# Performance work log

Measured on AMD Instinct MI355X. Metric: run time of the kernel, lower is better.

The kernel has to match this reference:

```python
import jax, jax.numpy as jnp
import numpy as np

N_HEAD = 8
D_MODEL = 512
D_K = 64
D_V = 64
LN_EPS = 1e-6


def setup_inputs() -> dict:
    key = jax.random.key(0)
    ks = jax.random.split(key, 8)
    B, L = 4, 1024
    inp = {
        "q": jax.random.normal(ks[0], (B, L, D_MODEL), dtype=jnp.float32),
        "k": jax.random.normal(ks[1], (B, L, D_MODEL), dtype=jnp.float32),
        "v": jax.random.normal(ks[2], (B, L, D_MODEL), dtype=jnp.float32),
        "w_qs": jax.random.normal(ks[3], (D_MODEL, N_HEAD * D_K), dtype=jnp.float32) * 0.02,
        "w_ks": jax.random.normal(ks[4], (D_MODEL, N_HEAD * D_K), dtype=jnp.float32) * 0.02,
        "w_vs": jax.random.normal(ks[5], (D_MODEL, N_HEAD * D_V), dtype=jnp.float32) * 0.02,
        "w_sk": jax.random.normal(ks[6], (D_V, N_HEAD * D_V), dtype=jnp.float32) * 0.02,
        "w_fc": jax.random.normal(ks[7], (D_V, D_MODEL), dtype=jnp.float32) * 0.02,
        "ln_gamma": jnp.ones((D_MODEL,), dtype=jnp.float32),
        "ln_beta": jnp.zeros((D_MODEL,), dtype=jnp.float32),
    }
    return inp


def reference(q, k, v, w_qs, w_ks, w_vs, w_sk, w_fc, ln_gamma, ln_beta):
    B, Lq, _ = q.shape
    Lk = k.shape[1]
    temp = jnp.asarray(D_K ** 0.5, q.dtype)
    residual = q

    # QKV projections (bias=False), split heads: [B, H, L, d]
    qh = (q @ w_qs).reshape(B, Lq, N_HEAD, D_K).transpose(0, 2, 1, 3)
    kh = (k @ w_ks).reshape(B, Lk, N_HEAD, D_K).transpose(0, 2, 1, 3)
    vh = (v @ w_vs).reshape(B, Lk, N_HEAD, D_V).transpose(0, 2, 1, 3)

    # scaled dot-product attention (dropout in eval mode = identity)
    attn = jax.nn.softmax(jnp.einsum('bhqd,bhkd->bhqk', qh / temp, kh), axis=-1)
    o = jnp.einsum('bhqk,bhkd->bhqd', attn, vh)  # [B, H, Lq, D_V]

    # SPA: selective parallel attention head gating
    u = o.sum(axis=1)                       # [B, Lq, D_V]
    s = u.mean(axis=1)                      # adaptive avg pool over Lq -> [B, D_V]
    g = jax.nn.softmax((s @ w_sk).reshape(B, N_HEAD, D_V), axis=1)  # softmax over heads
    f = o * g[:, :, None, :]                # gate each head, broadcast over Lq
    qo = f.sum(axis=1)                      # sum heads -> [B, Lq, D_V]

    # fc + residual + LayerNorm (dropout eval = identity)
    out = qo @ w_fc + residual              # [B, Lq, D_MODEL]
    mu = out.mean(axis=-1, keepdims=True)
    var = out.var(axis=-1, keepdims=True)
    out = (out - mu) * jax.lax.rsqrt(var + LN_EPS) * ln_gamma + ln_beta
    return out, attn
```

## Files before the change

kernel.cpp:

```cpp
#include <hip/hip_runtime.h>
#include <hip/hip_bf16.h>
#include <cstdint>

#define NH 8
#define DM 512
#define DH 64
#define NB 4
#define SL 1024

typedef __attribute__((ext_vector_type(8))) short bf16x8;
typedef __attribute__((ext_vector_type(4))) float f32x4;
typedef __attribute__((ext_vector_type(4))) unsigned int u32x4;

static __device__ __forceinline__ float bf2f(short s) {
  union { unsigned int u; float f; } c;
  c.u = ((unsigned int)(unsigned short)s) << 16;
  return c.f;
}
static __device__ __forceinline__ unsigned short f2bfbits(float f) {
  union { float f; unsigned int u; } c; c.f = f;
  unsigned int lsb = (c.u >> 16) & 1u;
  unsigned int r = c.u + 0x7fffu + lsb;
  return (unsigned short)(r >> 16);
}

__global__ __launch_bounds__(256) void k_cvt_act(
    const float* __restrict__ q, const float* __restrict__ k, const float* __restrict__ v,
    ushort* __restrict__ qb, ushort* __restrict__ kb, ushort* __restrict__ vb) {
  int i = blockIdx.x * 256 + threadIdx.x;
  {
    float4 f = ((const float4*)q)[i];
    ushort4 r = { f2bfbits(f.x), f2bfbits(f.y), f2bfbits(f.z), f2bfbits(f.w) };
    *(ushort4*)(qb + 4 * i) = r;
  }
  {
    float4 f = ((const float4*)k)[i];
    ushort4 r = { f2bfbits(f.x), f2bfbits(f.y), f2bfbits(f.z), f2bfbits(f.w) };
    *(ushort4*)(kb + 4 * i) = r;
  }
  {
    float4 f = ((const float4*)v)[i];
    ushort4 r = { f2bfbits(f.x), f2bfbits(f.y), f2bfbits(f.z), f2bfbits(f.w) };
    *(ushort4*)(vb + 4 * i) = r;
  }
}

__global__ __launch_bounds__(256) void k_cvt_wT(
    const float* __restrict__ w0, const float* __restrict__ w1, const float* __restrict__ w2,
    ushort* __restrict__ o0, ushort* __restrict__ o1, ushort* __restrict__ o2) {
  __shared__ ushort tile[64][65];
  const float* src = blockIdx.z == 0 ? w0 : (blockIdx.z == 1 ? w1 : w2);
  ushort* dst = blockIdx.z == 0 ? o0 : (blockIdx.z == 1 ? o1 : o2);
  int k0 = blockIdx.x * 64, n0 = blockIdx.y * 64;
  int t = threadIdx.x;
  #pragma unroll
  for (int i = 0; i < 16; ++i) {
    int lin = t + i * 256, r = lin >> 6, c = lin & 63;
    tile[r][c] = f2bfbits(src[(size_t)(k0 + r) * DM + n0 + c]);
  }
  __syncthreads();
  #pragma unroll
  for (int i = 0; i < 16; ++i) {
    int lin = t + i * 256, r = lin >> 6, c = lin & 63;
    dst[(size_t)(n0 + r) * DM + k0 + c] = tile[c][r];
  }
}

__global__ __launch_bounds__(256) void k_cvt_wfc(const float* __restrict__ w, ushort* __restrict__ o) {
  int i = blockIdx.x * 256 + threadIdx.x;
  float4 f = ((const float4*)w)[i];
  ushort4 r = { f2bfbits(f.x), f2bfbits(f.y), f2bfbits(f.z), f2bfbits(f.w) };
  *(ushort4*)(o + 4 * i) = r;
}

__global__ __launch_bounds__(256) void k_proj(
    const ushort* __restrict__ qb, const ushort* __restrict__ kb, const ushort* __restrict__ vb,
    const ushort* __restrict__ wqT, const ushort* __restrict__ wkT, const ushort* __restrict__ wvT,
    ushort* __restrict__ Qh, ushort* __restrict__ Kh, ushort* __restrict__ VhT) {
  int z = blockIdx.z;
  const ushort* A = z == 0 ? qb : (z == 1 ? kb : vb);
  const ushort* W = z == 0 ? wqT : (z == 1 ? wkT : wvT);
  ushort* Out = z == 0 ? Qh : (z == 1 ? Kh : VhT);
  float scale = z == 0 ? 0.125f * 1.44269504088896f : 1.0f;

  int wid = threadIdx.x >> 6, l = threadIdx.x & 63;
  int lr = l & 15, lg = l >> 4;
  int row0 = blockIdx.x * 64 + wid * 16;
  int col0 = blockIdx.y * 64;
  const ushort* Arow = A + (size_t)(row0 + lr) * DM + lg * 8;

  f32x4 acc0 = {0.f, 0.f, 0.f, 0.f}, acc1 = acc0, acc2 = acc0, acc3 = acc0;
  #pragma unroll 4
  for (int kt = 0; kt < 16; ++kt) {
    bf16x8 a = *(const bf16x8*)(Arow + kt * 32);
    bf16x8 b0 = *(const bf16x8*)(W + (size_t)(col0 + 0 * 16 + lr) * DM + kt * 32 + lg * 8);
    bf16x8 b1 = *(const bf16x8*)(W + (size_t)(col0 + 1 * 16 + lr) * DM + kt * 32 + lg * 8);
    bf16x8 b2 = *(const bf16x8*)(W + (size_t)(col0 + 2 * 16 + lr) * DM + kt * 32 + lg * 8);
    bf16x8 b3 = *(const bf16x8*)(W + (size_t)(col0 + 3 * 16 + lr) * DM + kt * 32 + lg * 8);
    acc0 = __builtin_amdgcn_mfma_f32_16x16x32_bf16(a, b0, acc0, 0, 0, 0);
    acc1 = __builtin_amdgcn_mfma_f32_16x16x32_bf16(a, b1, acc1, 0, 0, 0);
    acc2 = __builtin_amdgcn_mfma_f32_16x16x32_bf16(a, b2, acc2, 0, 0, 0);
    acc3 = __builtin_amdgcn_mfma_f32_16x16x32_bf16(a, b3, acc3, 0, 0, 0);
  }
  f32x4 accs[4] = {acc0, acc1, acc2, acc3};
  #pragma unroll
  for (int ct = 0; ct < 4; ++ct) {
    int gcol = col0 + ct * 16 + lr;
    int h = gcol >> 6, d = gcol & 63;
    #pragma unroll
    for (int r = 0; r < 4; ++r) {
      int grow = row0 + lg * 4 + r;
      int bb = grow >> 10, li = grow & 1023;
      float val = accs[ct][r] * scale;
      size_t addr;
      if (z == 2) addr = ((size_t)((bb * NH + h) * DH + d)) * SL + li;
      else        addr = ((size_t)((bb * NH + h) * SL + li)) * DH + d;
      Out[addr] = f2bfbits(val);
    }
  }
}

__global__ __launch_bounds__(256, 2) void k_attn_flash(
    const ushort* __restrict__ Qh, const ushort* __restrict__ Kh,
    const ushort* __restrict__ VhT, float* __restrict__ O,
    float* __restrict__ invS) {
  __shared__ __align__(16) unsigned int Plds[4][2][320];

  int bid = blockIdx.x;
  int xcd = bid & 7;
  int loc = bid >> 3;
  int bh  = xcd * 4 + (loc >> 4);
  int wid = threadIdx.x >> 6, l = threadIdx.x & 63;
  int rt  = (loc & 15) * 4 + wid;
  int lr = l & 15, g = l >> 4;
  int q0 = rt * 16;

  const ushort* Qbase = Qh + ((size_t)(bh * SL + q0 + lr)) * DH + g * 8;
  bf16x8 bQ0 = *(const bf16x8*)(Qbase);
  bf16x8 bQ1 = *(const bf16x8*)(Qbase + 32);
  const ushort* Kbase = Kh + (size_t)bh * SL * DH + (size_t)lr * DH + g * 8;
  const ushort* Vbase = VhT + (size_t)bh * DH * SL;

  f32x4 o0 = {0.f, 0.f, 0.f, 0.f}, o1 = o0, o2 = o0, o3 = o0;
  float sacc = 0.f;

  #pragma unroll 2
  for (int kb = 0; kb < 32; ++kb) {
    unsigned int* Pw = &Plds[wid][kb & 1][0];
    #pragma unroll
    for (int c = 0; c < 2; ++c) {
      int k0 = kb * 32 + c * 16;
      const ushort* kp = Kbase + (size_t)k0 * DH;
      bf16x8 a0 = *(const bf16x8*)(kp);
      bf16x8 a1 = *(const bf16x8*)(kp + 32);
      f32x4 acc = {0.f, 0.f, 0.f, 0.f};
      acc = __builtin_amdgcn_mfma_f32_16x16x32_bf16(a0, bQ0, acc, 0, 0, 0);
      acc = __builtin_amdgcn_mfma_f32_16x16x32_bf16(a1, bQ1, acc, 0, 0, 0);
      float p0 = exp2f(acc[0]), p1 = exp2f(acc[1]);
      float p2 = exp2f(acc[2]), p3 = exp2f(acc[3]);
      sacc += (p0 + p1) + (p2 + p3);
      unsigned int pk0, pk1;
      asm("v_cvt_pk_bf16_f32 %0, %1, %2" : "=v"(pk0) : "v"(p0), "v"(p1));
      asm("v_cvt_pk_bf16_f32 %0, %1, %2" : "=v"(pk1) : "v"(p2), "v"(p3));
      uint2 w2 = { pk0, pk1 };
      *(uint2*)(Pw + lr * 20 + c * 8 + 2 * g) = w2;
    }
    union { u32x4 u; bf16x8 b; } ap;
    ap.u = *(u32x4*)(Pw + lr * 20 + 4 * g);
    #pragma unroll
    for (int dt = 0; dt < 4; ++dt) {
      bf16x8 bV = *(const bf16x8*)(Vbase + (size_t)(dt * 16 + lr) * SL + kb * 32 + g * 8);
      f32x4& oo = dt == 0 ? o0 : (dt == 1 ? o1 : (dt == 2 ? o2 : o3));
      oo = __builtin_amdgcn_mfma_f32_16x16x32_bf16(ap.b, bV, oo, 0, 0, 0);
    }
  }

  sacc += __shfl_xor(sacc, 16);
  sacc += __shfl_xor(sacc, 32);
  float inv = 1.0f / sacc;
  if (l < 16) invS[(size_t)bh * SL + q0 + l] = inv;

  float invr[4];
  #pragma unroll
  for (int r = 0; r < 4; ++r) invr[r] = __shfl(inv, 4 * g + r);

  f32x4 os[4] = { o0, o1, o2, o3 };
  #pragma unroll
  for (int dt = 0; dt < 4; ++dt)
    #pragma unroll
    for (int r = 0; r < 4; ++r)
      O[((size_t)(bh * SL + q0 + 4 * g + r)) * DH + dt * 16 + lr] = os[dt][r] * invr[r];
}

__global__ __launch_bounds__(256, 4) void k_attn_store(
    const ushort* __restrict__ Qh, const ushort* __restrict__ Kh,
    const float* __restrict__ invS, float* __restrict__ attn_out) {
  __shared__ __align__(16) ushort S[16 * 1024];
  char* Sb = (char*)S;

  int bid = blockIdx.x;
  int xcd = bid & 7;
  int loc = bid >> 3;
  int bh  = xcd * 4 + (loc >> 6);
  int rt  = loc & 63;
  int wid = threadIdx.x >> 6, l = threadIdx.x & 63;
  int lr = l & 15, g = l >> 4;
  int q0 = rt * 16;

  const ushort* Qbase = Qh + ((size_t)(bh * SL + q0 + lr)) * DH + g * 8;
  bf16x8 bQ0 = *(const bf16x8*)(Qbase);
  bf16x8 bQ1 = *(const bf16x8*)(Qbase + 32);
  const ushort* Kbase = Kh + (size_t)bh * SL * DH + (size_t)lr * DH + g * 8;
  float invq = invS[(size_t)bh * SL + q0 + lr];

  #pragma unroll 4
  for (int ct = 0; ct < 16; ++ct) {
    int k0 = wid * 256 + ct * 16;
    const ushort* kp = Kbase + (size_t)k0 * DH;
    bf16x8 a0 = *(const bf16x8*)(kp);
    bf16x8 a1 = *(const bf16x8*)(kp + 32);
    f32x4 acc = {0.f, 0.f, 0.f, 0.f};
    acc = __builtin_amdgcn_mfma_f32_16x16x32_bf16(a0, bQ0, acc, 0, 0, 0);
    acc = __builtin_amdgcn_mfma_f32_16x16x32_bf16(a1, bQ1, acc, 0, 0, 0);
    float p0 = exp2f(acc[0]) * invq, p1 = exp2f(acc[1]) * invq;
    float p2 = exp2f(acc[2]) * invq, p3 = exp2f(acc[3]) * invq;
    unsigned int pk0, pk1;
    asm("v_cvt_pk_bf16_f32 %0, %1, %2" : "=v"(pk0) : "v"(p0), "v"(p1));
    asm("v_cvt_pk_bf16_f32 %0, %1, %2" : "=v"(pk1) : "v"(p2), "v"(p3));
    uint2 w2 = { pk0, pk1 };
    *(uint2*)(Sb + ((lr * 2048 + (k0 + 4 * g) * 2) ^ ((lr & 7) << 4))) = w2;
  }
  __syncthreads();

  size_t attn_base = (size_t)bh * SL * SL + (size_t)q0 * SL;
  #pragma unroll
  for (int rr = 0; rr < 4; ++rr) {
    int r = wid * 4 + rr;
    float* arow = attn_out + attn_base + (size_t)r * SL;
    #pragma unroll
    for (int i = 0; i < 4; ++i) {
      int c0 = 4 * l + 256 * i;
      uint2 u = *(uint2*)(Sb + ((r * 2048 + c0 * 2) ^ ((r & 7) << 4)));
      float4 pv;
      pv.x = bf2f((short)(u.x & 0xffff));
      pv.y = bf2f((short)(u.x >> 16));
      pv.z = bf2f((short)(u.y & 0xffff));
      pv.w = bf2f((short)(u.y >> 16));
      *(float4*)(arow + c0) = pv;
    }
  }
}

__global__ __launch_bounds__(256) void k_reduce(const float* __restrict__ O, float* __restrict__ partial) {
  int slab = blockIdx.x, bb = blockIdx.y;
  int d = threadIdx.x & 63, sub = threadIdx.x >> 6;
  float s = 0.f;
  for (int h = 0; h < NH; ++h) {
    const float* base = O + ((size_t)((bb * NH + h) * SL + slab * 32 + sub * 8)) * DH + d;
    #pragma unroll
    for (int li = 0; li < 8; ++li) s += base[(size_t)li * DH];
  }
  __shared__ float red[4][64];
  red[sub][d] = s;
  __syncthreads();
  if (threadIdx.x < 64) {
    float t = red[0][d] + red[1][d] + red[2][d] + red[3][d];
    partial[(bb * 32 + slab) * 64 + d] = t;
  }
}

__global__ __launch_bounds__(256) void k_gate(const float* __restrict__ partial,
                                              const float* __restrict__ wsk, float* __restrict__ g) {
  int bb = blockIdx.x;
  int t = threadIdx.x;
  __shared__ float red[4][64];
  __shared__ float sl[64];
  __shared__ float logit[512];
  int d = t & 63, q4 = t >> 6;
  float s = 0.f;
  for (int i = 0; i < 8; ++i) s += partial[(bb * 32 + q4 * 8 + i) * 64 + d];
  red[q4][d] = s;
  __syncthreads();
  if (t < 64) sl[t] = (red[0][t] + red[1][t] + red[2][t] + red[3][t]) * (1.0f / 1024.0f);
  __syncthreads();
  #pragma unroll
  for (int jj = 0; jj < 2; ++jj) {
    int j = t + jj * 256;
    float lg = 0.f;
    #pragma unroll 8
    for (int c = 0; c < 64; ++c) lg += sl[c] * wsk[c * DM + j];
    logit[j] = lg;
  }
  __syncthreads();
  if (t < 64) {
    float m = -1e30f;
    #pragma unroll
    for (int h = 0; h < NH; ++h) m = fmaxf(m, logit[h * 64 + t]);
    float sum = 0.f, e[NH];
    #pragma unroll
    for (int h = 0; h < NH; ++h) { e[h] = __expf(logit[h * 64 + t] - m); sum += e[h]; }
    float inv = 1.0f / sum;
    #pragma unroll
    for (int h = 0; h < NH; ++h) g[bb * DM + h * 64 + t] = e[h] * inv;
  }
}

__global__ __launch_bounds__(256) void k_final(
    const float* __restrict__ O, const float* __restrict__ g, const ushort* __restrict__ wfc,
    const float* __restrict__ q, const float* __restrict__ gamma, const float* __restrict__ beta,
    float* __restrict__ out) {
  __shared__ __align__(16) ushort wl[32768];
  __shared__ __align__(16) float qo[16][64];
  __shared__ __align__(16) float gl[512];
  int lt = blockIdx.x, bb = blockIdx.y;
  int t = threadIdx.x;

  gl[t] = g[bb * DM + t];
  gl[t + 256] = g[bb * DM + 256 + t];
  {
    int jg2 = t & 15, hi = t >> 4;
    #pragma unroll
    for (int m = 0; m < 16; ++m) {
      int di = m * 16 + hi;
      int d = di >> 2, i8 = di & 3;
      bf16x8 w8 = *(const bf16x8*)(wfc + d * DM + jg2 * 32 + i8 * 8);
      *(bf16x8*)(wl + (size_t)(d * 64 + i8 * 16 + jg2) * 8) = w8;
    }
  }
  __syncthreads();

  int r = t >> 4, jg = t & 15;
  int l = lt * 16 + r;
  {
    float4 acc; acc.x = acc.y = acc.z = acc.w = 0.f;
    #pragma unroll
    for (int h = 0; h < NH; ++h) {
      float4 ov = *(const float4*)(O + ((size_t)((bb * NH + h) * SL + l)) * DH + jg * 4);
      float4 gv = *(const float4*)(gl + h * 64 + jg * 4);
      acc.x += ov.x * gv.x; acc.y += ov.y * gv.y; acc.z += ov.z * gv.z; acc.w += ov.w * gv.w;
    }
    *(float4*)&qo[r][jg * 4] = acc;
  }
  __syncthreads();

  float val[32];
  const float* qrow = q + ((size_t)(bb * SL + l)) * DM + jg * 32;
  #pragma unroll
  for (int i4 = 0; i4 < 8; ++i4) *(float4*)&val[i4 * 4] = *(const float4*)(qrow + i4 * 4);

  for (int d = 0; d < 64; ++d) {
    float qd = qo[r][d];
    #pragma unroll
    for (int i8 = 0; i8 < 4; ++i8) {
      bf16x8 wv8 = *(const bf16x8*)(wl + (size_t)(d * 64 + i8 * 16 + jg) * 8);
      #pragma unroll
      for (int e = 0; e < 8; ++e) val[i8 * 8 + e] += qd * bf2f(wv8[e]);
    }
  }

  float s = 0.f, ss = 0.f;
  #pragma unroll
  for (int i = 0; i < 32; ++i) { s += val[i]; ss += val[i] * val[i]; }
  #pragma unroll
  for (int m = 1; m < 16; m <<= 1) { s += __shfl_xor(s, m, 16); ss += __shfl_xor(ss, m, 16); }
  float mu = s * (1.0f / 512.0f);
  float var = ss * (1.0f / 512.0f) - mu * mu;
  float rstd = rsqrtf(var + 1e-6f);

  float* orow = out + ((size_t)(bb * SL + l)) * DM + jg * 32;
  const float* gam = gamma + jg * 32;
  const float* bet = beta + jg * 32;
  #pragma unroll
  for (int i = 0; i < 32; ++i)
    orow[i] = (val[i] - mu) * rstd * gam[i] + bet[i];
}

extern "C" void kernel_launch(void* const* d_in, const int* in_sizes, int n_in,
                              void* d_out, int out_size, void* d_ws, size_t ws_size,
                              hipStream_t stream) {
  (void)in_sizes; (void)n_in; (void)out_size; (void)ws_size;
  const float* q     = (const float*)d_in[0];
  const float* k     = (const float*)d_in[1];
  const float* v     = (const float*)d_in[2];
  const float* w_qs  = (const float*)d_in[3];
  const float* w_ks  = (const float*)d_in[4];
  const float* w_vs  = (const float*)d_in[5];
  const float* w_sk  = (const float*)d_in[6];
  const float* w_fc  = (const float*)d_in[7];
  const float* gamma = (const float*)d_in[8];
  const float* beta  = (const float*)d_in[9];

  float* out  = (float*)d_out;
  float* attn = out + (size_t)NB * SL * DM;

  char* wsb = (char*)d_ws;
  ushort* qb   = (ushort*)(wsb + 0);
  ushort* kb   = (ushort*)(wsb + 4194304);
  ushort* vb   = (ushort*)(wsb + 8388608);
  ushort* wqT  = (ushort*)(wsb + 12582912);
  ushort* wkT  = (ushort*)(wsb + 13107200);
  ushort* wvT  = (ushort*)(wsb + 13631488);
  ushort* wfcb = (ushort*)(wsb + 14155776);
  ushort* Qh   = (ushort*)(wsb + 14221312);
  ushort* Kh   = (ushort*)(wsb + 18415616);
  ushort* VhT  = (ushort*)(wsb + 22609920);
  float*  O    = (float*)(wsb + 26804224);
  float*  part = (float*)(wsb + 35192832);
  float*  gbuf = (float*)(wsb + 35225600);
  float*  invS = (float*)(wsb + 0);

  k_cvt_act<<<dim3(2048), dim3(256), 0, stream>>>(q, k, v, qb, kb, vb);
  k_cvt_wT<<<dim3(8, 8, 3), dim3(256), 0, stream>>>(w_qs, w_ks, w_vs, wqT, wkT, wvT);
  k_cvt_wfc<<<dim3(32), dim3(256), 0, stream>>>(w_fc, wfcb);
  k_proj<<<dim3(64, 8, 3), dim3(256), 0, stream>>>(qb, kb, vb, wqT, wkT, wvT, Qh, Kh, VhT);
  k_attn_flash<<<dim3(512), dim3(256), 0, stream>>>(Qh, Kh, VhT, O, invS);
  k_attn_store<<<dim3(2048), dim3(256), 0, stream>>>(Qh, Kh, invS, attn);
  k_reduce<<<dim3(32, 4), dim3(256), 0, stream>>>(O, part);
  k_gate<<<dim3(4), dim3(256), 0, stream>>>(part, w_sk, gbuf);
  k_final<<<dim3(64, 4), dim3(256), 0, stream>>>(O, gbuf, wfcb, q, gamma, beta, out);
}
```

Baseline: 202.4 us.

## Fuse flash attention and attention-matrix store into one kernel

Merges the separate attention-output kernel and the attention-probability store kernel into one kernel. Each block computes the full unnormalized probability row tile once into shared memory, reduces row sums across waves, writes the normalized attn matrix, then reuses the shared P tile for the P·V MFMA. This removes the duplicate QK^T and exp computation, the invS round trip and one launch. Each block now holds the P tile until P·V finishes, and P·V is done by one wave per 16-column slice, which may lower overlap.

Result: faster. 168.6 us (-16.7%).

```diff
diff --git a/kernel.cpp b/kernel.cpp
--- a/kernel.cpp
+++ b/kernel.cpp
@@ -10,7 +10,6 @@
 
 typedef __attribute__((ext_vector_type(8))) short bf16x8;
 typedef __attribute__((ext_vector_type(4))) float f32x4;
-typedef __attribute__((ext_vector_type(4))) unsigned int u32x4;
 
 static __device__ __forceinline__ float bf2f(short s) {
   union { unsigned int u; float f; } c;
@@ -120,82 +119,11 @@
   }
 }
 
-__global__ __launch_bounds__(256, 2) void k_attn_flash(
-    const ushort* __restrict__ Qh, const ushort* __restrict__ Kh,
-    const ushort* __restrict__ VhT, float* __restrict__ O,
-    float* __restrict__ invS) {
-  __shared__ __align__(16) unsigned int Plds[4][2][320];
-
-  int bid = blockIdx.x;
-  int xcd = bid & 7;
-  int loc = bid >> 3;
-  int bh  = xcd * 4 + (loc >> 4);
-  int wid = threadIdx.x >> 6, l = threadIdx.x & 63;
-  int rt  = (loc & 15) * 4 + wid;
-  int lr = l & 15, g = l >> 4;
-  int q0 = rt * 16;
-
-  const ushort* Qbase = Qh + ((size_t)(bh * SL + q0 + lr)) * DH + g * 8;
-  bf16x8 bQ0 = *(const bf16x8*)(Qbase);
-  bf16x8 bQ1 = *(const bf16x8*)(Qbase + 32);
-  const ushort* Kbase = Kh + (size_t)bh * SL * DH + (size_t)lr * DH + g * 8;
-  const ushort* Vbase = VhT + (size_t)bh * DH * SL;
-
-  f32x4 o0 = {0.f, 0.f, 0.f, 0.f}, o1 = o0, o2 = o0, o3 = o0;
-  float sacc = 0.f;
-
-  #pragma unroll 2
-  for (int kb = 0; kb < 32; ++kb) {
-    unsigned int* Pw = &Plds[wid][kb & 1][0];
-    #pragma unroll
-    for (int c = 0; c < 2; ++c) {
-      int k0 = kb * 32 + c * 16;
-      const ushort* kp = Kbase + (size_t)k0 * DH;
-      bf16x8 a0 = *(const bf16x8*)(kp);
-      bf16x8 a1 = *(const bf16x8*)(kp + 32);
-      f32x4 acc = {0.f, 0.f, 0.f, 0.f};
-      acc = __builtin_amdgcn_mfma_f32_16x16x32_bf16(a0, bQ0, acc, 0, 0, 0);
-      acc = __builtin_amdgcn_mfma_f32_16x16x32_bf16(a1, bQ1, acc, 0, 0, 0);
-      float p0 = exp2f(acc[0]), p1 = exp2f(acc[1]);
-      float p2 = exp2f(acc[2]), p3 = exp2f(acc[3]);
-      sacc += (p0 + p1) + (p2 + p3);
-      unsigned int pk0, pk1;
-      asm("v_cvt_pk_bf16_f32 %0, %1, %2" : "=v"(pk0) : "v"(p0), "v"(p1));
-      asm("v_cvt_pk_bf16_f32 %0, %1, %2" : "=v"(pk1) : "v"(p2), "v"(p3));
-      uint2 w2 = { pk0, pk1 };
-      *(uint2*)(Pw + lr * 20 + c * 8 + 2 * g) = w2;
-    }
-    union { u32x4 u; bf16x8 b; } ap;
-    ap.u = *(u32x4*)(Pw + lr * 20 + 4 * g);
-    #pragma unroll
-    for (int dt = 0; dt < 4; ++dt) {
-      bf16x8 bV = *(const bf16x8*)(Vbase + (size_t)(dt * 16 + lr) * SL + kb * 32 + g * 8);
-      f32x4& oo = dt == 0 ? o0 : (dt == 1 ? o1 : (dt == 2 ? o2 : o3));
-      oo = __builtin_amdgcn_mfma_f32_16x16x32_bf16(ap.b, bV, oo, 0, 0, 0);
-    }
-  }
-
-  sacc += __shfl_xor(sacc, 16);
-  sacc += __shfl_xor(sacc, 32);
-  float inv = 1.0f / sacc;
-  if (l < 16) invS[(size_t)bh * SL + q0 + l] = inv;
-
-  float invr[4];
-  #pragma unroll
-  for (int r = 0; r < 4; ++r) invr[r] = __shfl(inv, 4 * g + r);
-
-  f32x4 os[4] = { o0, o1, o2, o3 };
-  #pragma unroll
-  for (int dt = 0; dt < 4; ++dt)
-    #pragma unroll
-    for (int r = 0; r < 4; ++r)
-      O[((size_t)(bh * SL + q0 + 4 * g + r)) * DH + dt * 16 + lr] = os[dt][r] * invr[r];
-}
-
-__global__ __launch_bounds__(256, 4) void k_attn_store(
-    const ushort* __restrict__ Qh, const ushort* __restrict__ Kh,
-    const float* __restrict__ invS, float* __restrict__ attn_out) {
+__global__ __launch_bounds__(256, 4) void k_attn(
+    const ushort* __restrict__ Qh, const ushort* __restrict__ Kh, const ushort* __restrict__ VhT,
+    float* __restrict__ attn_out, float* __restrict__ O) {
   __shared__ __align__(16) ushort S[16 * 1024];
+  __shared__ float spart[4][16];
   char* Sb = (char*)S;
 
   int bid = blockIdx.x;
@@ -211,8 +139,8 @@
   bf16x8 bQ0 = *(const bf16x8*)(Qbase);
   bf16x8 bQ1 = *(const bf16x8*)(Qbase + 32);
   const ushort* Kbase = Kh + (size_t)bh * SL * DH + (size_t)lr * DH + g * 8;
-  float invq = invS[(size_t)bh * SL + q0 + lr];
-
+
+  float sacc = 0.f;
   #pragma unroll 4
   for (int ct = 0; ct < 16; ++ct) {
     int k0 = wid * 256 + ct * 16;
@@ -222,32 +150,52 @@
     f32x4 acc = {0.f, 0.f, 0.f, 0.f};
     acc = __builtin_amdgcn_mfma_f32_16x16x32_bf16(a0, bQ0, acc, 0, 0, 0);
     acc = __builtin_amdgcn_mfma_f32_16x16x32_bf16(a1, bQ1, acc, 0, 0, 0);
-    float p0 = exp2f(acc[0]) * invq, p1 = exp2f(acc[1]) * invq;
-    float p2 = exp2f(acc[2]) * invq, p3 = exp2f(acc[3]) * invq;
+    float p0 = exp2f(acc[0]), p1 = exp2f(acc[1]);
+    float p2 = exp2f(acc[2]), p3 = exp2f(acc[3]);
+    sacc += (p0 + p1) + (p2 + p3);
     unsigned int pk0, pk1;
     asm("v_cvt_pk_bf16_f32 %0, %1, %2" : "=v"(pk0) : "v"(p0), "v"(p1));
     asm("v_cvt_pk_bf16_f32 %0, %1, %2" : "=v"(pk1) : "v"(p2), "v"(p3));
     uint2 w2 = { pk0, pk1 };
-    *(uint2*)(Sb + ((lr * 2048 + (k0 + 4 * g) * 2) ^ ((lr & 7) << 4))) = w2;
-  }
+    *(uint2*)(Sb + (((lr << 11) + ((k0 + 4 * g) << 1)) ^ ((lr & 7) << 4))) = w2;
+  }
+  sacc += __shfl_xor(sacc, 16);
+  sacc += __shfl_xor(sacc, 32);
+  if (l < 16) spart[wid][l] = sacc;
   __syncthreads();
 
   size_t attn_base = (size_t)bh * SL * SL + (size_t)q0 * SL;
   #pragma unroll
   for (int rr = 0; rr < 4; ++rr) {
     int r = wid * 4 + rr;
+    float inv = 1.0f / (spart[0][r] + spart[1][r] + spart[2][r] + spart[3][r]);
     float* arow = attn_out + attn_base + (size_t)r * SL;
     #pragma unroll
     for (int i = 0; i < 4; ++i) {
       int c0 = 4 * l + 256 * i;
-      uint2 u = *(uint2*)(Sb + ((r * 2048 + c0 * 2) ^ ((r & 7) << 4)));
+      uint2 u = *(uint2*)(Sb + (((r << 11) + (c0 << 1)) ^ ((r & 7) << 4)));
       float4 pv;
-      pv.x = bf2f((short)(u.x & 0xffff));
-      pv.y = bf2f((short)(u.x >> 16));
-      pv.z = bf2f((short)(u.y & 0xffff));
-      pv.w = bf2f((short)(u.y >> 16));
+      pv.x = bf2f((short)(u.x & 0xffff)) * inv;
+      pv.y = bf2f((short)(u.x >> 16)) * inv;
+      pv.z = bf2f((short)(u.y & 0xffff)) * inv;
+      pv.w = bf2f((short)(u.y >> 16)) * inv;
       *(float4*)(arow + c0) = pv;
     }
+  }
+
+  const ushort* Vbase = VhT + (size_t)bh * DH * SL + (size_t)(wid * 16 + lr) * SL + g * 8;
+  f32x4 acc = {0.f, 0.f, 0.f, 0.f};
+  #pragma unroll 8
+  for (int kt = 0; kt < 32; ++kt) {
+    bf16x8 aP = *(const bf16x8*)(Sb + (((lr << 11) + ((kt * 32 + g * 8) << 1)) ^ ((lr & 7) << 4)));
+    bf16x8 bV = *(const bf16x8*)(Vbase + kt * 32);
+    acc = __builtin_amdgcn_mfma_f32_16x16x32_bf16(aP, bV, acc, 0, 0, 0);
+  }
+  #pragma unroll
+  for (int r = 0; r < 4; ++r) {
+    int qr = 4 * g + r;
+    float inv = 1.0f / (spart[0][qr] + spart[1][qr] + spart[2][qr] + spart[3][qr]);
+    O[((size_t)(bh * SL + q0 + qr)) * DH + wid * 16 + lr] = acc[r] * inv;
   }
 }
 
@@ -407,14 +355,12 @@
   float*  O    = (float*)(wsb + 26804224);
   float*  part = (float*)(wsb + 35192832);
   float*  gbuf = (float*)(wsb + 35225600);
-  float*  invS = (float*)(wsb + 0);
 
   k_cvt_act<<<dim3(2048), dim3(256), 0, stream>>>(q, k, v, qb, kb, vb);
   k_cvt_wT<<<dim3(8, 8, 3), dim3(256), 0, stream>>>(w_qs, w_ks, w_vs, wqT, wkT, wvT);
   k_cvt_wfc<<<dim3(32), dim3(256), 0, stream>>>(w_fc, wfcb);
   k_proj<<<dim3(64, 8, 3), dim3(256), 0, stream>>>(qb, kb, vb, wqT, wkT, wvT, Qh, Kh, VhT);
-  k_attn_flash<<<dim3(512), dim3(256), 0, stream>>>(Qh, Kh, VhT, O, invS);
-  k_attn_store<<<dim3(2048), dim3(256), 0, stream>>>(Qh, Kh, invS, attn);
+  k_attn<<<dim3(2048), dim3(256), 0, stream>>>(Qh, Kh, VhT, attn, O);
   k_reduce<<<dim3(32, 4), dim3(256), 0, stream>>>(O, part);
   k_gate<<<dim3(4), dim3(256), 0, stream>>>(part, w_sk, gbuf);
   k_final<<<dim3(64, 4), dim3(256), 0, stream>>>(O, gbuf, wfcb, q, gamma, beta, out);
```
